# Optimization experiments

Hardware: AMD Instinct MI355X
Metric: run time of the kernel (lower is better)

Reference implementation:

```python
import jax, jax.numpy as jnp
import numpy as np

EPS = 1e-12


def setup_inputs() -> dict:
    key = jax.random.key(0)
    k1, k2, k3, k4, k5, k6 = jax.random.split(key, 6)
    N, R, T, D, depth = 50000, 1000, 400000, 256, 2
    features = jax.random.normal(k1, (N, D), dtype=jnp.float32)
    rel_emb = jax.random.normal(k2, (R, D), dtype=jnp.float32)
    # xavier-style scale for [D,1] kernels, stored as [depth, D]
    attn_kernels = jax.random.normal(k3, (depth, D), dtype=jnp.float32) * np.sqrt(2.0 / (D + 1))
    r_val = jnp.ones((T,), dtype=jnp.float32)
    adj = jax.random.randint(k4, (2, T), 0, N, dtype=jnp.int64)
    r_index_tri = jnp.arange(T, dtype=jnp.int64)  # one relation per triple
    r_index_rel = jax.random.randint(k5, (T,), 0, R, dtype=jnp.int64)
    return {
        "features": features,
        "rel_emb": rel_emb,
        "attn_kernels": attn_kernels,
        "r_val": r_val,
        "adj": adj,
        "r_index_tri": r_index_tri,
        "r_index_rel": r_index_rel,
    }


def reference(features, rel_emb, attn_kernels, r_val, adj, r_index_tri, r_index_rel):
    N, D = features.shape
    T = adj.shape[1]
    depth = attn_kernels.shape[0]
    dst, src = adj[0], adj[1]  # softmax/aggregate over dst rows, gather neighbors via src

    x = jnp.tanh(features)
    outputs = [x]
    for l in range(depth):
        # sparse [T,R] @ rel_emb -> per-triple relation embedding [T, D]
        tri_rel = jax.ops.segment_sum(r_val[:, None] * rel_emb[r_index_rel], r_index_tri, num_segments=T)
        # L2 normalize per edge (torch F.normalize, eps=1e-12)
        norm = jnp.sqrt(jnp.sum(tri_rel * tri_rel, axis=1, keepdims=True))
        tri_rel = tri_rel / jnp.maximum(norm, EPS)
        # gather neighbor features and reflect across relation hyperplane
        neighs = x[src]  # [T, D]
        neighs = neighs - 2.0 * jnp.sum(neighs * tri_rel, axis=1, keepdims=True) * tri_rel
        # per-edge attention logits, segment softmax over destination rows
        att = tri_rel @ attn_kernels[l]  # [T]
        seg_max = jax.ops.segment_max(att, dst, num_segments=N)  # [N]
        e = jnp.exp(att - seg_max[dst])
        seg_sum = jax.ops.segment_sum(e, dst, num_segments=N)
        w = e / seg_sum[dst]  # [T]
        # scatter-sum weighted neighbor messages
        new_features = jax.ops.segment_sum(neighs * w[:, None], dst, num_segments=N)
        x = jnp.tanh(new_features)
        outputs.append(x)
    return jnp.concatenate(outputs, axis=-1)  # [N, D*(depth+1)]
```

## Files before the change

kernel.cpp:

```cpp
#include <hip/hip_runtime.h>
#include <hip/hip_bf16.h>
#include <hip/hip_fp16.h>

static constexpr int kN = 50000;
static constexpr int kR = 1000;
static constexpr int kT = 400000;
static constexpr int kD = 256;
static constexpr int kOutD = 768;
static constexpr int kNB = (kN + 255) / 256;

static constexpr size_t kOffRel16 = 2219008;
static constexpr size_t kOffXb1   = 2752512;
static constexpr size_t kXbBytes  = (size_t)kN * kD * 2;
static constexpr size_t kWsNeed   = kOffXb1 + kXbBytes;
static constexpr int kShRowB = 3072;
static constexpr int kShOffB = 2048;

#define EPS_NORM 1e-12f

typedef unsigned int u32;
typedef unsigned long long u64;
typedef u32 u32x2_t __attribute__((ext_vector_type(2)));
typedef u32 u32x4_t __attribute__((ext_vector_type(4)));

__device__ __forceinline__ float bf2f(__hip_bfloat16 h) { return __bfloat162float(h); }

__device__ __forceinline__ float4 cvt8(u32x2_t u) {
  float4 f;
  f.x = __half2float(__ushort_as_half((unsigned short)(u.x & 0xFFFFu)));
  f.y = __half2float(__ushort_as_half((unsigned short)(u.x >> 16)));
  f.z = __half2float(__ushort_as_half((unsigned short)(u.y & 0xFFFFu)));
  f.w = __half2float(__ushort_as_half((unsigned short)(u.y >> 16)));
  return f;
}
__device__ __forceinline__ float4 asf4(u32x4_t u) {
  float4 f;
  f.x = __uint_as_float(u.x); f.y = __uint_as_float(u.y);
  f.z = __uint_as_float(u.z); f.w = __uint_as_float(u.w);
  return f;
}

__device__ __forceinline__ u32x2_t gload8(u64 sbase, u32 voff) {
  u32x2_t r;
  asm volatile("global_load_dwordx2 %0, %1, %2"
               : "=v"(r) : "v"(voff), "s"(sbase) : "memory");
  return r;
}
__device__ __forceinline__ u32x4_t gload16(u64 sbase, u32 voff) {
  u32x4_t r;
  asm volatile("global_load_dwordx4 %0, %1, %2"
               : "=v"(r) : "v"(voff), "s"(sbase) : "memory");
  return r;
}
__device__ __forceinline__ void waitv0() {
  asm volatile("s_waitcnt vmcnt(0)" ::: "memory");
  __builtin_amdgcn_sched_barrier(0);
}

__device__ __forceinline__ float loadF(const void* p, int i, int f32m) {
  return f32m ? ((const float*)p)[i] : bf2f(((const __hip_bfloat16*)p)[i]);
}
__device__ __forceinline__ int loadI(const void* p, int i, int i64m) {
  return i64m ? (int)(((const long long*)p)[i]) : ((const int*)p)[i];
}

__global__ void __launch_bounds__(256) detect_kernel(
    const void* __restrict__ feat, const void* __restrict__ adj,
    int* __restrict__ flags) {
  __shared__ int s_f32, s_i64;
  if (threadIdx.x == 0) { s_f32 = 0; s_i64 = 1; }
  __syncthreads();
  const __hip_bfloat16* fb = (const __hip_bfloat16*)feat;
  for (int i = threadIdx.x; i < 4096; i += 256) {
    const float v = bf2f(fb[i]);
    if (!(fabsf(v) <= 64.f)) atomicExch(&s_f32, 1);
  }
  const int* ai = (const int*)adj;
  for (int i = threadIdx.x; i < 2048; i += 256) {
    if (ai[2 * i + 1] != 0) atomicExch(&s_i64, 0);
  }
  __syncthreads();
  if (threadIdx.x == 0) { flags[0] = s_f32; flags[1] = s_i64; }
}

__global__ void __launch_bounds__(256) relnorm_kernel(
    const void* __restrict__ rel_emb, const void* __restrict__ attn_k,
    __half* __restrict__ rel16, float* __restrict__ attL,
    const int* __restrict__ flags) {
  const int f32m = flags[0];
  const int r = blockIdx.x;
  const int d = threadIdx.x;
  const float v  = loadF(rel_emb, r * kD + d, f32m);
  const float k0 = loadF(attn_k, d, f32m);
  const float k1 = loadF(attn_k, kD + d, f32m);
  float ss = v * v, d0 = v * k0, d1 = v * k1;
#pragma unroll
  for (int off = 32; off > 0; off >>= 1) {
    ss += __shfl_xor(ss, off);
    d0 += __shfl_xor(d0, off);
    d1 += __shfl_xor(d1, off);
  }
  __shared__ float s_ss[4], s_d0[4], s_d1[4];
  const int wave = threadIdx.x >> 6, lane = threadIdx.x & 63;
  if (lane == 0) { s_ss[wave] = ss; s_d0[wave] = d0; s_d1[wave] = d1; }
  __syncthreads();
  const float tss = s_ss[0] + s_ss[1] + s_ss[2] + s_ss[3];
  const float inv = 1.0f / fmaxf(sqrtf(tss), EPS_NORM);
  rel16[r * kD + d] = __float2half(v * inv);
  if (threadIdx.x == 0) {
    attL[r]      = (s_d0[0] + s_d0[1] + s_d0[2] + s_d0[3]) * inv;
    attL[kR + r] = (s_d1[0] + s_d1[1] + s_d1[2] + s_d1[3]) * inv;
  }
}

__global__ void __launch_bounds__(256) x0_kernel(
    const void* __restrict__ feat, float* __restrict__ out,
    const int* __restrict__ flags) {
  const int f32m = flags[0];
  const int i4 = (blockIdx.x * 256 + threadIdx.x) * 4;
  float v0, v1, v2, v3;
  if (f32m) {
    const float4 f = ((const float4*)feat)[i4 >> 2];
    v0 = f.x; v1 = f.y; v2 = f.z; v3 = f.w;
  } else {
    union { ushort4 u; __hip_bfloat16 h[4]; } xu;
    xu.u = ((const ushort4*)feat)[i4 >> 2];
    v0 = bf2f(xu.h[0]); v1 = bf2f(xu.h[1]); v2 = bf2f(xu.h[2]); v3 = bf2f(xu.h[3]);
  }
  const int n = i4 >> 8, d = i4 & 255;
  float4 o; o.x = tanhf(v0); o.y = tanhf(v1); o.z = tanhf(v2); o.w = tanhf(v3);
  *(float4*)(out + (size_t)n * kOutD + d) = o;
  ushort4 h;
  h.x = __half_as_ushort(__float2half(o.x));
  h.y = __half_as_ushort(__float2half(o.y));
  h.z = __half_as_ushort(__float2half(o.z));
  h.w = __half_as_ushort(__float2half(o.w));
  *(ushort4*)((char*)out + (size_t)n * kShRowB + kShOffB + (size_t)d * 2) = h;
}

__global__ void __launch_bounds__(256) count_kernel(
    const void* __restrict__ adj, int* __restrict__ counts,
    const int* __restrict__ flags) {
  const int t = blockIdx.x * 256 + threadIdx.x;
  if (t >= kT) return;
  atomicAdd(&counts[loadI(adj, t, flags[1])], 1);
}

__global__ void __launch_bounds__(256) psum_kernel(
    const int* __restrict__ counts, int* __restrict__ partials) {
  const int i = blockIdx.x * 256 + threadIdx.x;
  int v = (i < kN) ? counts[i] : 0;
#pragma unroll
  for (int off = 32; off > 0; off >>= 1) v += __shfl_xor(v, off);
  __shared__ int sw[4];
  const int lane = threadIdx.x & 63, wv = threadIdx.x >> 6;
  if (lane == 0) sw[wv] = v;
  __syncthreads();
  if (threadIdx.x == 0) partials[blockIdx.x] = sw[0] + sw[1] + sw[2] + sw[3];
}

__global__ void __launch_bounds__(256) pscan_kernel(int* __restrict__ partials) {
  const int tid = threadIdx.x, lane = tid & 63, wv = tid >> 6;
  const int v = (tid < kNB) ? partials[tid] : 0;
  int x = v;
#pragma unroll
  for (int d = 1; d < 64; d <<= 1) {
    const int y = __shfl_up(x, d);
    if (lane >= d) x += y;
  }
  __shared__ int sw[4];
  if (lane == 63) sw[wv] = x;
  __syncthreads();
  int woff = 0;
  for (int w = 0; w < wv; ++w) woff += sw[w];
  if (tid < kNB) partials[tid] = woff + x - v;
}

__global__ void __launch_bounds__(256) offs_kernel(
    const int* __restrict__ counts, const int* __restrict__ partials,
    int* __restrict__ offsets, int* __restrict__ cursor) {
  const int i = blockIdx.x * 256 + threadIdx.x;
  const int lane = threadIdx.x & 63, wv = threadIdx.x >> 6;
  const int v = (i < kN) ? counts[i] : 0;
  int x = v;
#pragma unroll
  for (int d = 1; d < 64; d <<= 1) {
    const int y = __shfl_up(x, d);
    if (lane >= d) x += y;
  }
  __shared__ int sw[4];
  if (lane == 63) sw[wv] = x;
  __syncthreads();
  int woff = 0;
  for (int w = 0; w < wv; ++w) woff += sw[w];
  const int excl = partials[blockIdx.x] + woff + x - v;
  if (i < kN) { offsets[i] = excl; cursor[i] = excl; }
  if (i == 0) offsets[kN] = kT;
}

__global__ void __launch_bounds__(256) fill_kernel(
    const void* __restrict__ adj, const void* __restrict__ rrel,
    const void* __restrict__ r_val, int* __restrict__ cursor,
    int* __restrict__ perm, const int* __restrict__ flags) {
  const int t = blockIdx.x * 256 + threadIdx.x;
  if (t >= kT) return;
  const int f32m = flags[0], i64m = flags[1];
  const int dn = loadI(adj, t, i64m);
  const int sn = loadI(adj, kT + t, i64m);
  const int r  = loadI(rrel, t, i64m);
  const float rv = loadF(r_val, t, f32m);
  const int pk = (sn & 0xFFFF) | ((r & 0x3FF) << 16) |
                 ((rv != 0.f) ? (1 << 26) : 0) | ((rv < 0.f) ? (1 << 27) : 0);
  perm[atomicAdd(&cursor[dn], 1)] = pk;
}

template <int XF16, int XROWB, int XOFFB>
__global__ void __launch_bounds__(256, 5) layer_kernel(
    const int* __restrict__ offsets, const int* __restrict__ perm,
    const float* __restrict__ xin,
    const char* __restrict__ xb,
    const __half* __restrict__ rel16, const float* __restrict__ attL_l,
    float* __restrict__ out, int col0,
    __half* __restrict__ xbout) {
  const int lane = threadIdx.x & 63;
  const int n = blockIdx.x * 4 + (threadIdx.x >> 6);
  const int beg = offsets[n];
  const int cnt = offsets[n + 1] - beg;
  float4 acc = make_float4(0.f, 0.f, 0.f, 0.f);
  float* orow = out + (size_t)n * kOutD + col0;

  if (cnt > 0 && cnt <= 64) {
    int pk_l = 0;
    float logit = -1e30f;
    if (lane < cnt) {
      pk_l = perm[beg + lane];
      const float a = attL_l[(pk_l >> 16) & 0x3FF];
      const float sa = (pk_l & (1 << 27)) ? -a : a;
      logit = (pk_l & (1 << 26)) ? sa : 0.f;
    }
    asm volatile("" : "+v"(logit));

    const u32 voffx = (u32)lane * (XF16 ? 8u : 16u);
    const u32 voffr = (u32)lane * 8u;
    u32x2_t ux2[8]; u32x4_t ux4[8]; u32x2_t ur[8];

#define ISSUE_BATCH(BASE)                                                      \
  _Pragma("unroll") for (int k = 0; k < 8; ++k) {                              \
    const u32 p = (u32)__builtin_amdgcn_readlane(pk_l, (BASE) + k);            \
    if (XF16) {                                                                \
      ux2[k] = gload8((u64)xb + (u64)((p & 0xFFFFu) * (u32)XROWB) + (u32)XOFFB,\
                      voffx);                                                  \
    } else {                                                                   \
      ux4[k] = gload16((u64)xin + (u64)((p & 0xFFFFu) * 3072u) + 1024u, voffx);\
    }                                                                          \
    ur[k] = gload8((u64)rel16 + (u64)(((p >> 16) & 0x3FFu) << 9), voffr);      \
  }

#define COMPUTE_BATCH(BASE)                                                    \
  {                                                                            \
    float dt[8];                                                               \
    _Pragma("unroll") for (int k = 0; k < 8; ++k) {                            \
      const float sw = __uint_as_float(                                        \
          (u32)__builtin_amdgcn_readlane(__float_as_uint(w_me), (BASE) + k));  \
      float4 xv;                                                               \
      if (XF16) xv = cvt8(ux2[k]); else xv = asf4(ux4[k]);                     \
      const float4 rr = cvt8(ur[k]);                                           \
      dt[k] = xv.x * rr.x + xv.y * rr.y + xv.z * rr.z + xv.w * rr.w;           \
      acc.x += xv.x * sw; acc.y += xv.y * sw;                                  \
      acc.z += xv.z * sw; acc.w += xv.w * sw;                                  \
    }                                                                          \
    _Pragma("unroll") for (int off = 32; off > 0; off >>= 1) {                 \
      _Pragma("unroll") for (int k = 0; k < 8; ++k)                            \
        dt[k] += __shfl_xor(dt[k], off);                                       \
    }                                                                          \
    _Pragma("unroll") for (int k = 0; k < 8; ++k) {                            \
      const u32 p = (u32)__builtin_amdgcn_readlane(pk_l, (BASE) + k);          \
      const float sw = __uint_as_float(                                        \
          (u32)__builtin_amdgcn_readlane(__float_as_uint(w_me), (BASE) + k));  \
      const float cw = ((p >> 26) & 1u) ? (2.f * sw * dt[k]) : 0.f;            \
      const float4 rr = cvt8(ur[k]);                                           \
      acc.x -= cw * rr.x; acc.y -= cw * rr.y;                                  \
      acc.z -= cw * rr.z; acc.w -= cw * rr.w;                                  \
    }                                                                          \
  }

    ISSUE_BATCH(0);

    float m = logit;
    for (int off = 1; off < cnt; off <<= 1) m = fmaxf(m, __shfl_xor(m, off));
    const float e = (lane < cnt) ? __expf(logit - m) : 0.f;
    float s = e;
    for (int off = 1; off < cnt; off <<= 1) s += __shfl_xor(s, off);
    const float w_me = (lane < cnt) ? e / s : 0.f;

    int base = 0;
    while (true) {
      waitv0();
      COMPUTE_BATCH(base);
      base += 8;
      if (base >= cnt) break;
      ISSUE_BATCH(base);
    }
#undef ISSUE_BATCH
#undef COMPUTE_BATCH
  } else if (cnt > 64) {
    float lm = -1e30f;
    for (int i = lane; i < cnt; i += 64) {
      const int p = perm[beg + i];
      const float a = attL_l[(p >> 16) & 0x3FF];
      const float sa = (p & (1 << 27)) ? -a : a;
      lm = fmaxf(lm, (p & (1 << 26)) ? sa : 0.f);
    }
#pragma unroll
    for (int off = 32; off > 0; off >>= 1) lm = fmaxf(lm, __shfl_xor(lm, off));
    float ls = 0.f;
    for (int i = lane; i < cnt; i += 64) {
      const int p = perm[beg + i];
      const float a = attL_l[(p >> 16) & 0x3FF];
      const float sa = (p & (1 << 27)) ? -a : a;
      ls += __expf(((p & (1 << 26)) ? sa : 0.f) - lm);
    }
#pragma unroll
    for (int off = 32; off > 0; off >>= 1) ls += __shfl_xor(ls, off);
    const float inv_s = 1.f / ls;

    for (int base = 0; base < cnt; base += 64) {
      const int nIn = min(64, cnt - base);
      int pkl = 0; float wl = 0.f;
      if (lane < nIn) {
        pkl = perm[beg + base + lane];
        const float a = attL_l[(pkl >> 16) & 0x3FF];
        const float sa = (pkl & (1 << 27)) ? -a : a;
        wl = __expf(((pkl & (1 << 26)) ? sa : 0.f) - lm) * inv_s;
      }
      for (int k = 0; k < nIn; ++k) {
        const int p   = __shfl(pkl, k);
        const float w = __shfl(wl, k);
        float4 xv;
        if (XF16) {
          xv = cvt8(*(const u32x2_t*)(xb + (size_t)(p & 0xFFFF) * XROWB +
                                      XOFFB + (size_t)lane * 8));
        } else {
          xv = *(const float4*)((const char*)xin + (size_t)(p & 0xFFFF) * 3072 +
                                1024 + (size_t)lane * 16);
        }
        const float4 rr = cvt8(*(const u32x2_t*)((const char*)rel16 +
                               (((size_t)(p >> 16) & 0x3FF) << 9) +
                               (size_t)lane * 8));
        float dot = xv.x * rr.x + xv.y * rr.y + xv.z * rr.z + xv.w * rr.w;
#pragma unroll
        for (int off = 32; off > 0; off >>= 1) dot += __shfl_xor(dot, off);
        const float s2 = (p >> 26) & 1 ? 1.f : 0.f;
        const float c = 2.f * s2 * dot * w;
        acc.x += xv.x * w - c * rr.x;
        acc.y += xv.y * w - c * rr.y;
        acc.z += xv.z * w - c * rr.z;
        acc.w += xv.w * w - c * rr.w;
      }
    }
  }

  acc.x = tanhf(acc.x); acc.y = tanhf(acc.y);
  acc.z = tanhf(acc.z); acc.w = tanhf(acc.w);
  *(float4*)(orow + lane * 4) = acc;
  if (xbout) {
    ushort4 h;
    h.x = __half_as_ushort(__float2half(acc.x));
    h.y = __half_as_ushort(__float2half(acc.y));
    h.z = __half_as_ushort(__float2half(acc.z));
    h.w = __half_as_ushort(__float2half(acc.w));
    *(ushort4*)(xbout + (size_t)n * kD + lane * 4) = h;
  }
}

extern "C" void kernel_launch(void* const* d_in, const int* in_sizes, int n_in,
                              void* d_out, int out_size, void* d_ws, size_t ws_size,
                              hipStream_t stream) {
  const void* features = d_in[0];
  const void* rel_emb  = d_in[1];
  const void* attn_k   = d_in[2];
  const void* r_val    = d_in[3];
  const void* adj      = d_in[4];
  const void* rrel     = d_in[6];
  float* out           = (float*)d_out;

  char* ws = (char*)d_ws;
  int*    flags    = (int*)(ws + 0);
  float*  attL     = (float*)(ws + 4096);
  int*    partials = (int*)(ws + 12288);
  int*    counts   = (int*)(ws + 16384);
  int*    offsets  = (int*)(ws + 217088);
  int*    cursor   = (int*)(ws + 417792);
  int*    perm     = (int*)(ws + 618496);
  __half* rel16    = (__half*)(ws + kOffRel16);
  const bool full = (ws_size >= kWsNeed);
  __half* xb1 = full ? (__half*)(ws + kOffXb1) : nullptr;

  const int tb = (kT + 255) / 256;

  detect_kernel<<<1, 256, 0, stream>>>(features, adj, flags);
  relnorm_kernel<<<kR, 256, 0, stream>>>(rel_emb, attn_k, rel16, attL, flags);
  x0_kernel<<<kN * kD / 1024, 256, 0, stream>>>(features, out, flags);

  hipMemsetAsync(counts, 0, (size_t)kN * 4, stream);
  count_kernel<<<tb, 256, 0, stream>>>(adj, counts, flags);
  psum_kernel<<<kNB, 256, 0, stream>>>(counts, partials);
  pscan_kernel<<<1, 256, 0, stream>>>(partials);
  offs_kernel<<<kNB, 256, 0, stream>>>(counts, partials, offsets, cursor);
  fill_kernel<<<tb, 256, 0, stream>>>(adj, rrel, r_val, cursor, perm, flags);

  layer_kernel<1, kShRowB, kShOffB><<<kN / 4, 256, 0, stream>>>(
      offsets, perm, nullptr, (const char*)out, rel16, attL, out, kD, xb1);
  if (full) {
    layer_kernel<1, 512, 0><<<kN / 4, 256, 0, stream>>>(
        offsets, perm, nullptr, (const char*)xb1, rel16, attL + kR, out,
        2 * kD, nullptr);
  } else {
    layer_kernel<0, 1, 0><<<kN / 4, 256, 0, stream>>>(
        offsets, perm, out, nullptr, rel16, attL + kR, out, 2 * kD, nullptr);
  }
}
```

Baseline: 389.2 us.

## Merge preprocessing kernels and use DPP reductions in layer kernel

Combines the detection and count-zeroing steps into one kernel, and the relation normalization, x0 tanh and edge counting into a single prep launch. The partial scan is folded into the offsets kernel, which cuts the launch count from roughly nine to six. In the layer kernel, the per-edge dot-product and softmax reductions switch from shfl_xor to DPP row shifts plus ds_swizzle, and the packed indices and weights are cached instead of being read twice. Launch and sync overhead should drop, at the cost of each offs2 block re-summing its preceding partials and extra registers in the inner loop.

Measured after the change: 358.2 us. 1.09x faster.

```diff
diff --git a/kernel.cpp b/kernel.cpp
--- a/kernel.cpp
+++ b/kernel.cpp
@@ -8,6 +8,8 @@
 static constexpr int kD = 256;
 static constexpr int kOutD = 768;
 static constexpr int kNB = (kN + 255) / 256;
+static constexpr int kX0B = kN * kD / 1024;
+static constexpr int kTB = (kT + 255) / 256;
 
 static constexpr size_t kOffRel16 = 2219008;
 static constexpr size_t kOffXb1   = 2752512;
@@ -40,6 +42,16 @@
   return f;
 }
 
+template <int CTRL>
+__device__ __forceinline__ float dppmov(float x) {
+  return __uint_as_float((u32)__builtin_amdgcn_update_dpp(
+      0, (int)__float_as_uint(x), CTRL, 0xF, 0xF, false));
+}
+__device__ __forceinline__ float swz16(float x) {
+  return __uint_as_float((u32)__builtin_amdgcn_ds_swizzle(
+      (int)__float_as_uint(x), 0x401F));
+}
+
 __device__ __forceinline__ u32x2_t gload8(u64 sbase, u32 voff) {
   u32x2_t r;
   asm volatile("global_load_dwordx2 %0, %1, %2"
@@ -64,86 +76,85 @@
   return i64m ? (int)(((const long long*)p)[i]) : ((const int*)p)[i];
 }
 
-__global__ void __launch_bounds__(256) detect_kernel(
+__global__ void __launch_bounds__(256) detect_zero_kernel(
     const void* __restrict__ feat, const void* __restrict__ adj,
-    int* __restrict__ flags) {
-  __shared__ int s_f32, s_i64;
-  if (threadIdx.x == 0) { s_f32 = 0; s_i64 = 1; }
-  __syncthreads();
-  const __hip_bfloat16* fb = (const __hip_bfloat16*)feat;
-  for (int i = threadIdx.x; i < 4096; i += 256) {
-    const float v = bf2f(fb[i]);
-    if (!(fabsf(v) <= 64.f)) atomicExch(&s_f32, 1);
-  }
-  const int* ai = (const int*)adj;
-  for (int i = threadIdx.x; i < 2048; i += 256) {
-    if (ai[2 * i + 1] != 0) atomicExch(&s_i64, 0);
-  }
-  __syncthreads();
-  if (threadIdx.x == 0) { flags[0] = s_f32; flags[1] = s_i64; }
-}
-
-__global__ void __launch_bounds__(256) relnorm_kernel(
+    int* __restrict__ flags, int* __restrict__ counts) {
+  if (blockIdx.x == 0) {
+    __shared__ int s_f32, s_i64;
+    if (threadIdx.x == 0) { s_f32 = 0; s_i64 = 1; }
+    __syncthreads();
+    const __hip_bfloat16* fb = (const __hip_bfloat16*)feat;
+    for (int i = threadIdx.x; i < 4096; i += 256) {
+      const float v = bf2f(fb[i]);
+      if (!(fabsf(v) <= 64.f)) atomicExch(&s_f32, 1);
+    }
+    const int* ai = (const int*)adj;
+    for (int i = threadIdx.x; i < 2048; i += 256) {
+      if (ai[2 * i + 1] != 0) atomicExch(&s_i64, 0);
+    }
+    __syncthreads();
+    if (threadIdx.x == 0) { flags[0] = s_f32; flags[1] = s_i64; }
+  } else {
+    const int i = (blockIdx.x - 1) * 256 + threadIdx.x;
+    if (i < kN) counts[i] = 0;
+  }
+}
+
+__global__ void __launch_bounds__(256) prep_kernel(
     const void* __restrict__ rel_emb, const void* __restrict__ attn_k,
     __half* __restrict__ rel16, float* __restrict__ attL,
+    const void* __restrict__ feat, float* __restrict__ out,
+    const void* __restrict__ adj, int* __restrict__ counts,
     const int* __restrict__ flags) {
   const int f32m = flags[0];
-  const int r = blockIdx.x;
-  const int d = threadIdx.x;
-  const float v  = loadF(rel_emb, r * kD + d, f32m);
-  const float k0 = loadF(attn_k, d, f32m);
-  const float k1 = loadF(attn_k, kD + d, f32m);
-  float ss = v * v, d0 = v * k0, d1 = v * k1;
-#pragma unroll
-  for (int off = 32; off > 0; off >>= 1) {
-    ss += __shfl_xor(ss, off);
-    d0 += __shfl_xor(d0, off);
-    d1 += __shfl_xor(d1, off);
-  }
-  __shared__ float s_ss[4], s_d0[4], s_d1[4];
-  const int wave = threadIdx.x >> 6, lane = threadIdx.x & 63;
-  if (lane == 0) { s_ss[wave] = ss; s_d0[wave] = d0; s_d1[wave] = d1; }
-  __syncthreads();
-  const float tss = s_ss[0] + s_ss[1] + s_ss[2] + s_ss[3];
-  const float inv = 1.0f / fmaxf(sqrtf(tss), EPS_NORM);
-  rel16[r * kD + d] = __float2half(v * inv);
-  if (threadIdx.x == 0) {
-    attL[r]      = (s_d0[0] + s_d0[1] + s_d0[2] + s_d0[3]) * inv;
-    attL[kR + r] = (s_d1[0] + s_d1[1] + s_d1[2] + s_d1[3]) * inv;
-  }
-}
-
-__global__ void __launch_bounds__(256) x0_kernel(
-    const void* __restrict__ feat, float* __restrict__ out,
-    const int* __restrict__ flags) {
-  const int f32m = flags[0];
-  const int i4 = (blockIdx.x * 256 + threadIdx.x) * 4;
-  float v0, v1, v2, v3;
-  if (f32m) {
-    const float4 f = ((const float4*)feat)[i4 >> 2];
-    v0 = f.x; v1 = f.y; v2 = f.z; v3 = f.w;
+  const int b = blockIdx.x;
+  if (b < kR) {
+    const int r = b, d = threadIdx.x;
+    const float v  = loadF(rel_emb, r * kD + d, f32m);
+    const float k0 = loadF(attn_k, d, f32m);
+    const float k1 = loadF(attn_k, kD + d, f32m);
+    float ss = v * v, d0 = v * k0, d1 = v * k1;
+#pragma unroll
+    for (int off = 32; off > 0; off >>= 1) {
+      ss += __shfl_xor(ss, off);
+      d0 += __shfl_xor(d0, off);
+      d1 += __shfl_xor(d1, off);
+    }
+    __shared__ float s_ss[4], s_d0[4], s_d1[4];
+    const int wave = threadIdx.x >> 6, lane = threadIdx.x & 63;
+    if (lane == 0) { s_ss[wave] = ss; s_d0[wave] = d0; s_d1[wave] = d1; }
+    __syncthreads();
+    const float tss = s_ss[0] + s_ss[1] + s_ss[2] + s_ss[3];
+    const float inv = 1.0f / fmaxf(sqrtf(tss), EPS_NORM);
+    rel16[r * kD + d] = __float2half(v * inv);
+    if (threadIdx.x == 0) {
+      attL[r]      = (s_d0[0] + s_d0[1] + s_d0[2] + s_d0[3]) * inv;
+      attL[kR + r] = (s_d1[0] + s_d1[1] + s_d1[2] + s_d1[3]) * inv;
+    }
+  } else if (b < kR + kX0B) {
+    const int i4 = ((b - kR) * 256 + threadIdx.x) * 4;
+    float v0, v1, v2, v3;
+    if (f32m) {
+      const float4 f = ((const float4*)feat)[i4 >> 2];
+      v0 = f.x; v1 = f.y; v2 = f.z; v3 = f.w;
+    } else {
+      union { ushort4 u; __hip_bfloat16 h[4]; } xu;
+      xu.u = ((const ushort4*)feat)[i4 >> 2];
+      v0 = bf2f(xu.h[0]); v1 = bf2f(xu.h[1]); v2 = bf2f(xu.h[2]); v3 = bf2f(xu.h[3]);
+    }
+    const int n = i4 >> 8, d = i4 & 255;
+    float4 o; o.x = tanhf(v0); o.y = tanhf(v1); o.z = tanhf(v2); o.w = tanhf(v3);
+    *(float4*)(out + (size_t)n * kOutD + d) = o;
+    ushort4 h;
+    h.x = __half_as_ushort(__float2half(o.x));
+    h.y = __half_as_ushort(__float2half(o.y));
+    h.z = __half_as_ushort(__float2half(o.z));
+    h.w = __half_as_ushort(__float2half(o.w));
+    *(ushort4*)((char*)out + (size_t)n * kShRowB + kShOffB + (size_t)d * 2) = h;
   } else {
-    union { ushort4 u; __hip_bfloat16 h[4]; } xu;
-    xu.u = ((const ushort4*)feat)[i4 >> 2];
-    v0 = bf2f(xu.h[0]); v1 = bf2f(xu.h[1]); v2 = bf2f(xu.h[2]); v3 = bf2f(xu.h[3]);
-  }
-  const int n = i4 >> 8, d = i4 & 255;
-  float4 o; o.x = tanhf(v0); o.y = tanhf(v1); o.z = tanhf(v2); o.w = tanhf(v3);
-  *(float4*)(out + (size_t)n * kOutD + d) = o;
-  ushort4 h;
-  h.x = __half_as_ushort(__float2half(o.x));
-  h.y = __half_as_ushort(__float2half(o.y));
-  h.z = __half_as_ushort(__float2half(o.z));
-  h.w = __half_as_ushort(__float2half(o.w));
-  *(ushort4*)((char*)out + (size_t)n * kShRowB + kShOffB + (size_t)d * 2) = h;
-}
-
-__global__ void __launch_bounds__(256) count_kernel(
-    const void* __restrict__ adj, int* __restrict__ counts,
-    const int* __restrict__ flags) {
-  const int t = blockIdx.x * 256 + threadIdx.x;
-  if (t >= kT) return;
-  atomicAdd(&counts[loadI(adj, t, flags[1])], 1);
+    const int t = (b - kR - kX0B) * 256 + threadIdx.x;
+    if (t < kT) atomicAdd(&counts[loadI(adj, t, flags[1])], 1);
+  }
 }
 
 __global__ void __launch_bounds__(256) psum_kernel(
@@ -159,41 +170,31 @@
   if (threadIdx.x == 0) partials[blockIdx.x] = sw[0] + sw[1] + sw[2] + sw[3];
 }
 
-__global__ void __launch_bounds__(256) pscan_kernel(int* __restrict__ partials) {
-  const int tid = threadIdx.x, lane = tid & 63, wv = tid >> 6;
-  const int v = (tid < kNB) ? partials[tid] : 0;
+__global__ void __launch_bounds__(256) offs2_kernel(
+    const int* __restrict__ counts, const int* __restrict__ partials,
+    int* __restrict__ offsets, int* __restrict__ cursor) {
+  const int t = threadIdx.x, lane = t & 63, wv = t >> 6;
+  int pv = (t < (int)blockIdx.x) ? partials[t] : 0;
+#pragma unroll
+  for (int off = 32; off > 0; off >>= 1) pv += __shfl_xor(pv, off);
+  __shared__ int sb[4];
+  if (lane == 0) sb[wv] = pv;
+  __syncthreads();
+  const int pbase = sb[0] + sb[1] + sb[2] + sb[3];
+  const int i = blockIdx.x * 256 + t;
+  const int v = (i < kN) ? counts[i] : 0;
   int x = v;
 #pragma unroll
   for (int d = 1; d < 64; d <<= 1) {
     const int y = __shfl_up(x, d);
     if (lane >= d) x += y;
   }
-  __shared__ int sw[4];
-  if (lane == 63) sw[wv] = x;
+  __shared__ int sw2[4];
+  if (lane == 63) sw2[wv] = x;
   __syncthreads();
   int woff = 0;
-  for (int w = 0; w < wv; ++w) woff += sw[w];
-  if (tid < kNB) partials[tid] = woff + x - v;
-}
-
-__global__ void __launch_bounds__(256) offs_kernel(
-    const int* __restrict__ counts, const int* __restrict__ partials,
-    int* __restrict__ offsets, int* __restrict__ cursor) {
-  const int i = blockIdx.x * 256 + threadIdx.x;
-  const int lane = threadIdx.x & 63, wv = threadIdx.x >> 6;
-  const int v = (i < kN) ? counts[i] : 0;
-  int x = v;
-#pragma unroll
-  for (int d = 1; d < 64; d <<= 1) {
-    const int y = __shfl_up(x, d);
-    if (lane >= d) x += y;
-  }
-  __shared__ int sw[4];
-  if (lane == 63) sw[wv] = x;
-  __syncthreads();
-  int woff = 0;
-  for (int w = 0; w < wv; ++w) woff += sw[w];
-  const int excl = partials[blockIdx.x] + woff + x - v;
+  for (int w = 0; w < wv; ++w) woff += sw2[w];
+  const int excl = pbase + woff + x - v;
   if (i < kN) { offsets[i] = excl; cursor[i] = excl; }
   if (i == 0) offsets[kN] = kT;
 }
@@ -243,41 +244,45 @@
     const u32 voffx = (u32)lane * (XF16 ? 8u : 16u);
     const u32 voffr = (u32)lane * 8u;
     u32x2_t ux2[8]; u32x4_t ux4[8]; u32x2_t ur[8];
+    u32 pkk[8];
 
 #define ISSUE_BATCH(BASE)                                                      \
   _Pragma("unroll") for (int k = 0; k < 8; ++k) {                              \
-    const u32 p = (u32)__builtin_amdgcn_readlane(pk_l, (BASE) + k);            \
+    pkk[k] = (u32)__builtin_amdgcn_readlane(pk_l, (BASE) + k);                 \
     if (XF16) {                                                                \
-      ux2[k] = gload8((u64)xb + (u64)((p & 0xFFFFu) * (u32)XROWB) + (u32)XOFFB,\
-                      voffx);                                                  \
+      ux2[k] = gload8((u64)xb + (u64)((pkk[k] & 0xFFFFu) * (u32)XROWB) +       \
+                          (u32)XOFFB, voffx);                                  \
     } else {                                                                   \
-      ux4[k] = gload16((u64)xin + (u64)((p & 0xFFFFu) * 3072u) + 1024u, voffx);\
+      ux4[k] = gload16((u64)xin + (u64)((pkk[k] & 0xFFFFu) * 3072u) + 1024u,   \
+                       voffx);                                                 \
     }                                                                          \
-    ur[k] = gload8((u64)rel16 + (u64)(((p >> 16) & 0x3FFu) << 9), voffr);      \
+    ur[k] = gload8((u64)rel16 + (u64)(((pkk[k] >> 16) & 0x3FFu) << 9), voffr); \
   }
 
 #define COMPUTE_BATCH(BASE)                                                    \
   {                                                                            \
+    float wvv[8];                                                              \
+    _Pragma("unroll") for (int k = 0; k < 8; ++k)                              \
+      wvv[k] = __uint_as_float(                                                \
+          (u32)__builtin_amdgcn_readlane(__float_as_uint(w_me), (BASE) + k));  \
     float dt[8];                                                               \
     _Pragma("unroll") for (int k = 0; k < 8; ++k) {                            \
-      const float sw = __uint_as_float(                                        \
-          (u32)__builtin_amdgcn_readlane(__float_as_uint(w_me), (BASE) + k));  \
       float4 xv;                                                               \
       if (XF16) xv = cvt8(ux2[k]); else xv = asf4(ux4[k]);                     \
       const float4 rr = cvt8(ur[k]);                                           \
       dt[k] = xv.x * rr.x + xv.y * rr.y + xv.z * rr.z + xv.w * rr.w;           \
-      acc.x += xv.x * sw; acc.y += xv.y * sw;                                  \
-      acc.z += xv.z * sw; acc.w += xv.w * sw;                                  \
+      acc.x += xv.x * wvv[k]; acc.y += xv.y * wvv[k];                          \
+      acc.z += xv.z * wvv[k]; acc.w += xv.w * wvv[k];                          \
     }                                                                          \
-    _Pragma("unroll") for (int off = 32; off > 0; off >>= 1) {                 \
-      _Pragma("unroll") for (int k = 0; k < 8; ++k)                            \
-        dt[k] += __shfl_xor(dt[k], off);                                       \
-    }                                                                          \
+                            \
+    _Pragma("unroll") for (int k = 0; k < 8; ++k) dt[k] += dppmov<0x128>(dt[k]);\
+    _Pragma("unroll") for (int k = 0; k < 8; ++k) dt[k] += dppmov<0x124>(dt[k]);\
+    _Pragma("unroll") for (int k = 0; k < 8; ++k) dt[k] += dppmov<0x122>(dt[k]);\
+    _Pragma("unroll") for (int k = 0; k < 8; ++k) dt[k] += dppmov<0x121>(dt[k]);\
+    _Pragma("unroll") for (int k = 0; k < 8; ++k) dt[k] += swz16(dt[k]);       \
+    _Pragma("unroll") for (int k = 0; k < 8; ++k) dt[k] += __shfl_xor(dt[k], 32);\
     _Pragma("unroll") for (int k = 0; k < 8; ++k) {                            \
-      const u32 p = (u32)__builtin_amdgcn_readlane(pk_l, (BASE) + k);          \
-      const float sw = __uint_as_float(                                        \
-          (u32)__builtin_amdgcn_readlane(__float_as_uint(w_me), (BASE) + k));  \
-      const float cw = ((p >> 26) & 1u) ? (2.f * sw * dt[k]) : 0.f;            \
+      const float cw = ((pkk[k] >> 26) & 1u) ? (2.f * wvv[k] * dt[k]) : 0.f;   \
       const float4 rr = cvt8(ur[k]);                                           \
       acc.x -= cw * rr.x; acc.y -= cw * rr.y;                                  \
       acc.z -= cw * rr.z; acc.w -= cw * rr.w;                                  \
@@ -287,10 +292,20 @@
     ISSUE_BATCH(0);
 
     float m = logit;
-    for (int off = 1; off < cnt; off <<= 1) m = fmaxf(m, __shfl_xor(m, off));
+    m = fmaxf(m, dppmov<0x128>(m));
+    m = fmaxf(m, dppmov<0x124>(m));
+    m = fmaxf(m, dppmov<0x122>(m));
+    m = fmaxf(m, dppmov<0x121>(m));
+    if (cnt > 16) m = fmaxf(m, swz16(m));
+    if (cnt > 32) m = fmaxf(m, __shfl_xor(m, 32));
     const float e = (lane < cnt) ? __expf(logit - m) : 0.f;
     float s = e;
-    for (int off = 1; off < cnt; off <<= 1) s += __shfl_xor(s, off);
+    s += dppmov<0x128>(s);
+    s += dppmov<0x124>(s);
+    s += dppmov<0x122>(s);
+    s += dppmov<0x121>(s);
+    if (cnt > 16) s += swz16(s);
+    if (cnt > 32) s += __shfl_xor(s, 32);
     const float w_me = (lane < cnt) ? e / s : 0.f;
 
     int base = 0;
@@ -396,18 +411,12 @@
   const bool full = (ws_size >= kWsNeed);
   __half* xb1 = full ? (__half*)(ws + kOffXb1) : nullptr;
 
-  const int tb = (kT + 255) / 256;
-
-  detect_kernel<<<1, 256, 0, stream>>>(features, adj, flags);
-  relnorm_kernel<<<kR, 256, 0, stream>>>(rel_emb, attn_k, rel16, attL, flags);
-  x0_kernel<<<kN * kD / 1024, 256, 0, stream>>>(features, out, flags);
-
-  hipMemsetAsync(counts, 0, (size_t)kN * 4, stream);
-  count_kernel<<<tb, 256, 0, stream>>>(adj, counts, flags);
+  detect_zero_kernel<<<1 + kNB, 256, 0, stream>>>(features, adj, flags, counts);
+  prep_kernel<<<kR + kX0B + kTB, 256, 0, stream>>>(
+      rel_emb, attn_k, rel16, attL, features, out, adj, counts, flags);
   psum_kernel<<<kNB, 256, 0, stream>>>(counts, partials);
-  pscan_kernel<<<1, 256, 0, stream>>>(partials);
-  offs_kernel<<<kNB, 256, 0, stream>>>(counts, partials, offsets, cursor);
-  fill_kernel<<<tb, 256, 0, stream>>>(adj, rrel, r_val, cursor, perm, flags);
+  offs2_kernel<<<kNB, 256, 0, stream>>>(counts, partials, offsets, cursor);
+  fill_kernel<<<kTB, 256, 0, stream>>>(adj, rrel, r_val, cursor, perm, flags);
 
   layer_kernel<1, kShRowB, kShOffB><<<kN / 4, 256, 0, stream>>>(
       offsets, perm, nullptr, (const char*)out, rel16, attL, out, kD, xb1);
```
